# Kernel optimization log

Measured on AMD Instinct MI355X. Metric: run time of the kernel, lower is better.

## Reference

```python
import jax, jax.numpy as jnp
import numpy as np

N, D, H = 50000, 128, 2        # nodes, hidden_size(=ffn_size=out_channels), heads
E = 800000                      # edges
C = D                           # per-head out_channels (PyG TransformerConv)
EPS = 1e-5

def layer_norm(x, g, b):
    mu = jnp.mean(x, axis=-1, keepdims=True)
    var = jnp.mean((x - mu) ** 2, axis=-1, keepdims=True)
    return (x - mu) / jnp.sqrt(var + EPS) * g + b

def setup_inputs() -> dict:
    key = jax.random.key(0)
    ks = jax.random.split(key, 16)
    s_in = 1.0 / np.sqrt(D)
    s_ffn = 1.0 / np.sqrt(D)
    return {
        "x": jax.random.normal(ks[0], (N, D), jnp.float32),
        "edge_index": jax.random.randint(ks[1], (2, E), 0, N, jnp.int64),
        "ln1_g": jnp.ones((D,), jnp.float32),
        "ln1_b": jnp.zeros((D,), jnp.float32),
        "Wq": jax.random.normal(ks[2], (D, H * C), jnp.float32) * s_in,
        "bq": jnp.zeros((H * C,), jnp.float32),
        "Wk": jax.random.normal(ks[3], (D, H * C), jnp.float32) * s_in,
        "bk": jnp.zeros((H * C,), jnp.float32),
        "Wv": jax.random.normal(ks[4], (D, H * C), jnp.float32) * s_in,
        "bv": jnp.zeros((H * C,), jnp.float32),
        "Wskip": jax.random.normal(ks[5], (D, C), jnp.float32) * s_in,
        "bskip": jnp.zeros((C,), jnp.float32),
        "ln2_g": jnp.ones((D,), jnp.float32),
        "ln2_b": jnp.zeros((D,), jnp.float32),
        "W1": jax.random.normal(ks[6], (D, D), jnp.float32) * s_ffn,
        "b1": jnp.zeros((D,), jnp.float32),
        "W2": jax.random.normal(ks[7], (D, D), jnp.float32) * s_ffn,
        "b2": jnp.zeros((D,), jnp.float32),
    }

def reference(x, edge_index, ln1_g, ln1_b, Wq, bq, Wk, bk, Wv, bv,
              Wskip, bskip, ln2_g, ln2_b, W1, b1, W2, b2):
    src, dst = edge_index[0], edge_index[1]  # messages flow src(j) -> dst(i)
    n = x.shape[0]

    # --- self-attention block (pre-norm) ---
    y = layer_norm(x, ln1_g, ln1_b)
    q = (y @ Wq + bq).reshape(n, H, C)
    k = (y @ Wk + bk).reshape(n, H, C)
    v = (y @ Wv + bv).reshape(n, H, C)

    # per-edge attention logits [E, H]
    alpha = jnp.einsum('ehc,ehc->eh', q[dst], k[src]) / jnp.sqrt(jnp.float32(C))
    # softmax over incoming edges of each dst node
    m = jax.ops.segment_max(alpha, dst, num_segments=n)          # [N, H]
    p = jnp.exp(alpha - m[dst])                                  # [E, H]
    denom = jax.ops.segment_sum(p, dst, num_segments=n)          # [N, H]
    a = p / denom[dst]                                           # [E, H]

    attn = jax.ops.segment_sum(a[:, :, None] * v[src], dst, num_segments=n)  # [N,H,C]
    out = attn.mean(axis=1) + (y @ Wskip + bskip)  # concat=False mean + root skip
    x = x + out  # residual (dropout is identity at eval)

    # --- FFN block (pre-norm) ---
    h = layer_norm(x, ln2_g, ln2_b)
    h = jax.nn.gelu(h @ W1 + b1, approximate=False) @ W2 + b2
    return x + h
```

## Files before the change

kernel.cpp:

```cpp
#include <hip/hip_runtime.h>
#include <hip/hip_bf16.h>
#include <math.h>


typedef unsigned short u16;
using short8 = __attribute__((ext_vector_type(8))) short;
using f32x4  = __attribute__((ext_vector_type(4))) float;
using f32x2  = __attribute__((ext_vector_type(2))) float;

__device__ __forceinline__ float bf2f(u16 u) {
    return __uint_as_float(((unsigned int)u) << 16);
}
__device__ __forceinline__ u16 f2bf(float f) {
    __hip_bfloat16 h = __float2bfloat16(f);
    return __builtin_bit_cast(u16, h);
}
__device__ __forceinline__ float bfe(short8 v, int j) {
    return bf2f((u16)v[j]);
}
__device__ __forceinline__ void fp8x4_to_f32(int w, float* out) {
    f32x2 lo = __builtin_amdgcn_cvt_pk_f32_fp8(w, false);
    f32x2 hi = __builtin_amdgcn_cvt_pk_f32_fp8(w, true);
    out[0] = lo[0]; out[1] = lo[1]; out[2] = hi[0]; out[3] = hi[1];
}
__device__ __forceinline__ unsigned pack_fp8x4(float4 f) {
    unsigned w = 0;
    w = (unsigned)__builtin_amdgcn_cvt_pk_fp8_f32(f.x, f.y, (int)w, false);
    w = (unsigned)__builtin_amdgcn_cvt_pk_fp8_f32(f.z, f.w, (int)w, true);
    return w;
}

__global__ __launch_bounds__(256) void fused_prep_ln(
    const float* __restrict__ x, const float* __restrict__ ln1g,
    const float* __restrict__ ln1b,
    const float* __restrict__ Wq, const float* __restrict__ Wk,
    const float* __restrict__ Wv, const float* __restrict__ Ws,
    const float* __restrict__ W1, const float* __restrict__ W2,
    const float* __restrict__ bq, const float* __restrict__ bk,
    const float* __restrict__ bv, const float* __restrict__ bs,
    u16* __restrict__ wt, float* __restrict__ bc,
    u16* __restrict__ y, int* __restrict__ cnt, int n,
    const int* __restrict__ edst, int e, int histBlocks)
{
    if (blockIdx.x < (unsigned)histBlocks) {
        int stride = histBlocks * 256;
        for (int i = blockIdx.x * 256 + threadIdx.x; i < e; i += stride)
            atomicAdd(&cnt[edst[i]], 1);
        return;
    }
    int gsz = (gridDim.x - histBlocks) * 256;
    int gtid = (blockIdx.x - histBlocks) * 256 + threadIdx.x;

    for (int i = gtid; i < 147456 + 896; i += gsz) {
        if (i < 147456) {
            const float* W; int N; int base;
            if      (i <  32768) { W = Wq; N = 256; base = 0; }
            else if (i <  65536) { W = Wk; N = 256; base = 32768; }
            else if (i <  98304) { W = Wv; N = 256; base = 65536; }
            else if (i < 114688) { W = Ws; N = 128; base = 98304; }
            else if (i < 131072) { W = W1; N = 128; base = 114688; }
            else                 { W = W2; N = 128; base = 131072; }
            int j = i - base;
            int nIdx = j >> 7, k = j & 127;
            wt[i] = f2bf(W[(size_t)k * N + nIdx]);
        } else {
            int j = i - 147456;
            float v;
            if      (j < 256) v = bq[j];
            else if (j < 512) v = bk[j - 256];
            else if (j < 768) v = bv[j - 512];
            else              v = bs[j - 768];
            bc[j] = v;
        }
    }
    int lane = threadIdx.x & 63;
    int gw = gtid >> 6, nw = gsz >> 6;
    for (int row = gw; row < n; row += nw) {
        size_t base = (size_t)row * 128;
        float v0 = x[base + lane];
        float v1 = x[base + 64 + lane];
        float s1 = v0 + v1, s2 = v0 * v0 + v1 * v1;
        for (int o = 1; o <= 32; o <<= 1) {
            s1 += __shfl_xor(s1, o);
            s2 += __shfl_xor(s2, o);
        }
        float mu = s1 * (1.f / 128.f);
        float var = s2 * (1.f / 128.f) - mu * mu;
        float rstd = rsqrtf(var + 1e-5f);
        y[base + lane]      = f2bf((v0 - mu) * rstd * ln1g[lane] + ln1b[lane]);
        y[base + 64 + lane] = f2bf((v1 - mu) * rstd * ln1g[64 + lane] + ln1b[64 + lane]);
    }
}

__global__ __launch_bounds__(256) void scan_block_sum(const int* __restrict__ cnt,
                                                      int* __restrict__ bsum, int n) {
    __shared__ int s[256];
    int idx = blockIdx.x * 256 + threadIdx.x;
    s[threadIdx.x] = (idx < n) ? cnt[idx] : 0;
    __syncthreads();
    for (int o = 128; o > 0; o >>= 1) {
        if (threadIdx.x < o) s[threadIdx.x] += s[threadIdx.x + o];
        __syncthreads();
    }
    if (threadIdx.x == 0) bsum[blockIdx.x] = s[0];
}
__global__ __launch_bounds__(256) void scan_partials(const int* __restrict__ bsum,
                                                     int* __restrict__ bsumex, int nb) {
    __shared__ int s[256];
    int t = threadIdx.x;
    int v = (t < nb) ? bsum[t] : 0;
    s[t] = v;
    __syncthreads();
    for (int o = 1; o < 256; o <<= 1) {
        int add = (t >= o) ? s[t - o] : 0;
        __syncthreads();
        s[t] += add;
        __syncthreads();
    }
    bsumex[t] = s[t] - v;
}
__global__ __launch_bounds__(256) void scan_write(const int* __restrict__ cnt,
                                                  const int* __restrict__ bsumex,
                                                  int* __restrict__ rowptr,
                                                  int* __restrict__ cursor, int n, int etot) {
    __shared__ int s[256];
    int t = threadIdx.x;
    int idx = blockIdx.x * 256 + t;
    int v = (idx < n) ? cnt[idx] : 0;
    s[t] = v;
    __syncthreads();
    for (int o = 1; o < 256; o <<= 1) {
        int add = (t >= o) ? s[t - o] : 0;
        __syncthreads();
        s[t] += add;
        __syncthreads();
    }
    if (idx < n) {
        int ex = bsumex[blockIdx.x] + s[t] - v;
        rowptr[idx] = ex;
        cursor[idx] = ex;
    }
    if (idx == 0) rowptr[n] = etot;
}

__global__ __launch_bounds__(256, 3) void qkv_gemm(
    const u16* __restrict__ A, const u16* __restrict__ Bt,
    const float* __restrict__ bias, u16* __restrict__ qkv,
    float* __restrict__ skip, int n,
    const int* __restrict__ dst, const int* __restrict__ src,
    int* __restrict__ cursor, int* __restrict__ esrc, int e, int scatBlocks)
{
    __shared__ float wt4[4][32 * 66];
    if (blockIdx.x < (unsigned)scatBlocks) {
        int stride = scatBlocks * 256;
        for (int i = blockIdx.x * 256 + threadIdx.x; i < e; i += stride) {
            int p = atomicAdd(&cursor[dst[i]], 1);
            esrc[p] = src[i];
        }
        return;
    }
    int bid = blockIdx.x - scatBlocks;
    int wid = threadIdx.x >> 6, lane = threadIdx.x & 63;
    int wr = wid >> 1, wc = wid & 1;
    int r0 = bid * 64;
    int lm = lane & 15, quad = lane >> 4;
    float* wtile = wt4[wid];

    const u16* aBase = A + (size_t)(r0 + wr * 32 + lm) * 128 + quad * 8;
    short8 a0_0 = *(const short8*)(aBase + 0);
    short8 a0_1 = *(const short8*)(aBase + 32);
    short8 a0_2 = *(const short8*)(aBase + 64);
    short8 a0_3 = *(const short8*)(aBase + 96);
    short8 a1_0 = *(const short8*)(aBase + 16 * 128 + 0);
    short8 a1_1 = *(const short8*)(aBase + 16 * 128 + 32);
    short8 a1_2 = *(const short8*)(aBase + 16 * 128 + 64);
    short8 a1_3 = *(const short8*)(aBase + 16 * 128 + 96);

    int r = lane & 31, h = lane >> 5;
    int row = r0 + wr * 32 + r;
    bool rowOk = row < n;

    for (int by = 0; by < 7; ++by) {
        int c0 = by * 128;
        const u16* bBase = Bt + (size_t)(c0 + wc * 64 + lm) * 128 + quad * 8;
        f32x4 acc[2][4] = {};
#pragma unroll
        for (int kx = 0; kx < 4; ++kx) {
            short8 a0 = (kx == 0) ? a0_0 : (kx == 1) ? a0_1 : (kx == 2) ? a0_2 : a0_3;
            short8 a1 = (kx == 0) ? a1_0 : (kx == 1) ? a1_1 : (kx == 2) ? a1_2 : a1_3;
#pragma unroll
            for (int j = 0; j < 4; ++j) {
                short8 bj = *(const short8*)(bBase + (size_t)j * 16 * 128 + kx * 32);
                acc[0][j] = __builtin_amdgcn_mfma_f32_16x16x32_bf16(a0, bj, acc[0][j], 0, 0, 0);
                acc[1][j] = __builtin_amdgcn_mfma_f32_16x16x32_bf16(a1, bj, acc[1][j], 0, 0, 0);
            }
        }
#pragma unroll
        for (int j = 0; j < 4; ++j) {
            float bv = bias[c0 + wc * 64 + j * 16 + lm];
#pragma unroll
            for (int rt = 0; rt < 2; ++rt)
#pragma unroll
                for (int i2 = 0; i2 < 4; ++i2)
                    wtile[(rt * 16 + quad * 4 + i2) * 66 + j * 16 + lm]
                        = acc[rt][j][i2] + bv;
        }
        if (rowOk) {
            const float* wsrc = wtile + r * 66 + h * 32;
            int colW = wc * 64 + h * 32;
            if (c0 < 256) {
                u16* dp = qkv + (size_t)row * 640 + c0 + colW;
#pragma unroll
                for (int m2 = 0; m2 < 4; ++m2) {
                    short8 o;
#pragma unroll
                    for (int jj = 0; jj < 8; ++jj)
                        o[jj] = (short)f2bf(wsrc[m2 * 8 + jj]);
                    *(short8*)(dp + m2 * 8) = o;
                }
            } else if (c0 < 512) {
                unsigned char* kb = (unsigned char*)qkv + (size_t)row * 1280 + 512
                                    + (c0 - 256) + colW;
                uint4 w0, w1;
                w0.x = pack_fp8x4(make_float4(wsrc[0],  wsrc[1],  wsrc[2],  wsrc[3]));
                w0.y = pack_fp8x4(make_float4(wsrc[4],  wsrc[5],  wsrc[6],  wsrc[7]));
                w0.z = pack_fp8x4(make_float4(wsrc[8],  wsrc[9],  wsrc[10], wsrc[11]));
                w0.w = pack_fp8x4(make_float4(wsrc[12], wsrc[13], wsrc[14], wsrc[15]));
                w1.x = pack_fp8x4(make_float4(wsrc[16], wsrc[17], wsrc[18], wsrc[19]));
                w1.y = pack_fp8x4(make_float4(wsrc[20], wsrc[21], wsrc[22], wsrc[23]));
                w1.z = pack_fp8x4(make_float4(wsrc[24], wsrc[25], wsrc[26], wsrc[27]));
                w1.w = pack_fp8x4(make_float4(wsrc[28], wsrc[29], wsrc[30], wsrc[31]));
                *(uint4*)kb = w0;
                *(uint4*)(kb + 16) = w1;
            } else if (c0 < 768) {
                u16* dp = qkv + (size_t)row * 640 + 384 + (c0 - 512) + colW;
#pragma unroll
                for (int m2 = 0; m2 < 4; ++m2) {
                    short8 o;
#pragma unroll
                    for (int jj = 0; jj < 8; ++jj)
                        o[jj] = (short)f2bf(wsrc[m2 * 8 + jj]);
                    *(short8*)(dp + m2 * 8) = o;
                }
            } else {
                float* dp = skip + (size_t)row * 128 + colW;
#pragma unroll
                for (int m2 = 0; m2 < 8; ++m2)
                    *(float4*)(dp + m2 * 4) = *(const float4*)(wsrc + m2 * 4);
            }
        }
    }
}

__global__ __launch_bounds__(256) void attn_kernel(
    const u16* __restrict__ qkv, const int* __restrict__ rowptr,
    const int* __restrict__ esrc, const float* __restrict__ x,
    float* __restrict__ sx, const float* __restrict__ g2,
    const float* __restrict__ b2, u16* __restrict__ y, int n)
{
    int wid = threadIdx.x >> 6, lane = threadIdx.x & 63;
    int i = blockIdx.x * 4 + wid;
    if (i >= n) return;
    int slot = lane >> 5;
    int sub  = lane & 15;
    int colOff = ((lane >> 4) & 1) * 128 + sub * 8;

    const float scale = 0.08838834764831845f;
    short8 q8 = *(const short8*)(qkv + (size_t)i * 640 + colOff);
    float qf[8];
#pragma unroll
    for (int j = 0; j < 8; ++j) qf[j] = bfe(q8, j) * scale;

    int beg = rowptr[i], end = rowptr[i + 1];
    float l = 0.f;
    float acc[8] = {};

    int t = beg + slot;
    for (; t + 6 < end; t += 8) {
        int s0 = esrc[t], s1 = esrc[t + 2], s2 = esrc[t + 4], s3 = esrc[t + 6];
        const u16* n0 = qkv + (size_t)s0 * 640;
        const u16* n1 = qkv + (size_t)s1 * 640;
        const u16* n2 = qkv + (size_t)s2 * 640;
        const u16* n3 = qkv + (size_t)s3 * 640;
        uint2 kw0 = *(const uint2*)((const unsigned char*)(n0 + 256) + colOff);
        uint2 kw1 = *(const uint2*)((const unsigned char*)(n1 + 256) + colOff);
        uint2 kw2 = *(const uint2*)((const unsigned char*)(n2 + 256) + colOff);
        uint2 kw3 = *(const uint2*)((const unsigned char*)(n3 + 256) + colOff);
        short8 v0 = *(const short8*)(n0 + 384 + colOff);
        short8 v1 = *(const short8*)(n1 + 384 + colOff);
        short8 v2 = *(const short8*)(n2 + 384 + colOff);
        short8 v3 = *(const short8*)(n3 + 384 + colOff);
        float k0f[8], k1f[8], k2f[8], k3f[8];
        fp8x4_to_f32((int)kw0.x, k0f); fp8x4_to_f32((int)kw0.y, k0f + 4);
        fp8x4_to_f32((int)kw1.x, k1f); fp8x4_to_f32((int)kw1.y, k1f + 4);
        fp8x4_to_f32((int)kw2.x, k2f); fp8x4_to_f32((int)kw2.y, k2f + 4);
        fp8x4_to_f32((int)kw3.x, k3f); fp8x4_to_f32((int)kw3.y, k3f + 4);
        float d0 = 0.f, d1 = 0.f, d2 = 0.f, d3 = 0.f;
#pragma unroll
        for (int j = 0; j < 8; ++j) {
            d0 += qf[j] * k0f[j];
            d1 += qf[j] * k1f[j];
            d2 += qf[j] * k2f[j];
            d3 += qf[j] * k3f[j];
        }
#pragma unroll
        for (int o = 1; o <= 8; o <<= 1) {
            d0 += __shfl_xor(d0, o);
            d1 += __shfl_xor(d1, o);
            d2 += __shfl_xor(d2, o);
            d3 += __shfl_xor(d3, o);
        }
        float w0 = __expf(d0), w1 = __expf(d1);
        float w2 = __expf(d2), w3 = __expf(d3);
        l += w0 + w1 + w2 + w3;
#pragma unroll
        for (int j = 0; j < 8; ++j)
            acc[j] += w0 * bfe(v0, j) + w1 * bfe(v1, j)
                    + w2 * bfe(v2, j) + w3 * bfe(v3, j);
    }
    for (; t < end; t += 2) {
        int s0 = esrc[t];
        const u16* n0 = qkv + (size_t)s0 * 640;
        uint2 kw0 = *(const uint2*)((const unsigned char*)(n0 + 256) + colOff);
        short8 v0 = *(const short8*)(n0 + 384 + colOff);
        float k0f[8];
        fp8x4_to_f32((int)kw0.x, k0f); fp8x4_to_f32((int)kw0.y, k0f + 4);
        float d0 = 0.f;
#pragma unroll
        for (int j = 0; j < 8; ++j) d0 += qf[j] * k0f[j];
#pragma unroll
        for (int o = 1; o <= 8; o <<= 1) d0 += __shfl_xor(d0, o);
        float w0 = __expf(d0);
        l += w0;
#pragma unroll
        for (int j = 0; j < 8; ++j) acc[j] += w0 * bfe(v0, j);
    }

    l += __shfl_xor(l, 32);
    float inv = (l > 0.f) ? (1.f / l) : 0.f;
#pragma unroll
    for (int j = 0; j < 8; ++j) {
        acc[j] = (acc[j] + __shfl_xor(acc[j], 32)) * inv;
        acc[j] = 0.5f * (acc[j] + __shfl_xor(acc[j], 16));
    }

    if (lane < 16) {
        size_t base = (size_t)i * 128 + sub * 8;
        float4 xv0 = *(const float4*)(x + base);
        float4 xv1 = *(const float4*)(x + base + 4);
        float4 sk0 = *(const float4*)(sx + base);
        float4 sk1 = *(const float4*)(sx + base + 4);
        float r[8];
        r[0] = xv0.x + sk0.x + acc[0]; r[1] = xv0.y + sk0.y + acc[1];
        r[2] = xv0.z + sk0.z + acc[2]; r[3] = xv0.w + sk0.w + acc[3];
        r[4] = xv1.x + sk1.x + acc[4]; r[5] = xv1.y + sk1.y + acc[5];
        r[6] = xv1.z + sk1.z + acc[6]; r[7] = xv1.w + sk1.w + acc[7];
        *(float4*)(sx + base)     = make_float4(r[0], r[1], r[2], r[3]);
        *(float4*)(sx + base + 4) = make_float4(r[4], r[5], r[6], r[7]);
        float s1 = 0.f, s2 = 0.f;
#pragma unroll
        for (int j = 0; j < 8; ++j) { s1 += r[j]; s2 += r[j] * r[j]; }
#pragma unroll
        for (int o = 1; o <= 8; o <<= 1) {
            s1 += __shfl_xor(s1, o);
            s2 += __shfl_xor(s2, o);
        }
        float mu = s1 * (1.f / 128.f);
        float var = s2 * (1.f / 128.f) - mu * mu;
        float rstd = rsqrtf(var + 1e-5f);
        short8 o8;
#pragma unroll
        for (int j = 0; j < 8; ++j)
            o8[j] = (short)f2bf((r[j] - mu) * rstd * g2[sub * 8 + j] + b2[sub * 8 + j]);
        *(short8*)(y + base) = o8;
    }
}

__global__ __launch_bounds__(256) void ffn_kernel(
    const u16* __restrict__ y2, const u16* __restrict__ W1T,
    const float* __restrict__ b1, const u16* __restrict__ W2T,
    const float* __restrict__ b2, const float* __restrict__ x2,
    float* __restrict__ out, int n)
{
    __shared__ u16 t1[64 * 136];
    int wid = threadIdx.x >> 6, lane = threadIdx.x & 63;
    int lm = lane & 15, quad = lane >> 4;
    int r0 = blockIdx.x * 64 + wid * 16;

    const u16* aBase = y2 + (size_t)(r0 + lm) * 128 + quad * 8;
    f32x4 acc[8] = {};
#pragma unroll
    for (int kk = 0; kk < 128; kk += 32) {
        short8 a0 = *(const short8*)(aBase + kk);
#pragma unroll
        for (int j = 0; j < 8; ++j) {
            short8 bj = *(const short8*)(W1T + (size_t)(j * 16 + lm) * 128 + quad * 8 + kk);
            acc[j] = __builtin_amdgcn_mfma_f32_16x16x32_bf16(a0, bj, acc[j], 0, 0, 0);
        }
    }
#pragma unroll
    for (int j = 0; j < 8; ++j) {
        int col = j * 16 + lm;
        float bv = b1[col];
#pragma unroll
        for (int i2 = 0; i2 < 4; ++i2) {
            int rl = wid * 16 + quad * 4 + i2;
            float v = acc[j][i2] + bv;
            v = 0.5f * v * (1.f + erff(v * 0.70710678118654752f));
            t1[rl * 136 + col] = f2bf(v);
        }
    }
    __syncthreads();

    f32x4 acc2[8] = {};
#pragma unroll
    for (int kk = 0; kk < 128; kk += 32) {
        short8 a0 = *(const short8*)(t1 + (wid * 16 + lm) * 136 + quad * 8 + kk);
#pragma unroll
        for (int j = 0; j < 8; ++j) {
            short8 bj = *(const short8*)(W2T + (size_t)(j * 16 + lm) * 128 + quad * 8 + kk);
            acc2[j] = __builtin_amdgcn_mfma_f32_16x16x32_bf16(a0, bj, acc2[j], 0, 0, 0);
        }
    }
#pragma unroll
    for (int j = 0; j < 8; ++j) {
        int col = j * 16 + lm;
        float bv = b2[col];
#pragma unroll
        for (int i2 = 0; i2 < 4; ++i2) {
            int row = r0 + quad * 4 + i2;
            if (row >= n) continue;
            size_t ob = (size_t)row * 128 + col;
            out[ob] = acc2[j][i2] + bv + x2[ob];
        }
    }
}

extern "C" void kernel_launch(void* const* d_in, const int* in_sizes, int n_in,
                              void* d_out, int out_size, void* d_ws, size_t ws_size,
                              hipStream_t stream)
{
    const float* x    = (const float*)d_in[0];
    const int*   ei   = (const int*)d_in[1];

    int n = in_sizes[0] / 128;
    int e = in_sizes[1] / 2;
    const int* src  = ei;
    const int* dstp = ei + e;

    char* w = (char*)d_ws;
    size_t off = 0;
    auto alloc = [&](size_t bytes) -> void* {
        void* p = w + off;
        off = (off + bytes + 255) & ~(size_t)255;
        return p;
    };
    u16*   y    = (u16*)alloc((size_t)n * 128 * 2);
    u16*   qkv  = (u16*)alloc((size_t)n * 640 * 2);
    float* sx   = (float*)alloc((size_t)n * 128 * 4);
    u16*   wt   = (u16*)alloc((size_t)147456 * 2);
    float* bc   = (float*)alloc(896 * 4);
    int* cnt    = (int*)alloc((size_t)n * 4);
    int* cursor = (int*)alloc((size_t)n * 4);
    int* rowptr = (int*)alloc(((size_t)n + 1) * 4);
    int* esrc   = (int*)alloc((size_t)e * 4);
    int* bsum   = (int*)alloc(1024);
    int* bsumex = (int*)alloc(1024);

    int gr  = (n + 63) / 64;
    int nb  = (n + 255) / 256;
    int scatBlocks = 512;
    int histBlocks = 512;

    hipMemsetAsync(cnt, 0, (size_t)n * sizeof(int), stream);
    fused_prep_ln<<<2048 + histBlocks, 256, 0, stream>>>(
        x, (const float*)d_in[2], (const float*)d_in[3],
        (const float*)d_in[4], (const float*)d_in[6], (const float*)d_in[8],
        (const float*)d_in[10], (const float*)d_in[14], (const float*)d_in[16],
        (const float*)d_in[5], (const float*)d_in[7], (const float*)d_in[9],
        (const float*)d_in[11], wt, bc, y, cnt, n, dstp, e, histBlocks);
    scan_block_sum<<<nb, 256, 0, stream>>>(cnt, bsum, n);
    scan_partials<<<1, 256, 0, stream>>>(bsum, bsumex, nb);
    scan_write<<<nb, 256, 0, stream>>>(cnt, bsumex, rowptr, cursor, n, e);
    qkv_gemm<<<scatBlocks + gr, 256, 0, stream>>>(
        y, wt, bc, qkv, sx, n, dstp, src, cursor, esrc, e, scatBlocks);
    attn_kernel<<<(n + 3) / 4, 256, 0, stream>>>(qkv, rowptr, esrc, x, sx,
                                                 (const float*)d_in[12],
                                                 (const float*)d_in[13], y, n);
    ffn_kernel<<<gr, 256, 0, stream>>>(y, wt + 114688, (const float*)d_in[15],
                                       wt + 131072, (const float*)d_in[17],
                                       sx, (float*)d_out, n);
}
```

Measured before the change: 397.4 us.

## Stage A tile in LDS, bf16 epilogue tile, and unroll edge scatter in qkv_gemm

```diff
diff --git a/kernel.cpp b/kernel.cpp
--- a/kernel.cpp
+++ b/kernel.cpp
@@ -143,17 +143,30 @@
     if (idx == 0) rowptr[n] = etot;
 }
 
-__global__ __launch_bounds__(256, 3) void qkv_gemm(
+__global__ __launch_bounds__(256, 4) void qkv_gemm(
     const u16* __restrict__ A, const u16* __restrict__ Bt,
     const float* __restrict__ bias, u16* __restrict__ qkv,
     float* __restrict__ skip, int n,
     const int* __restrict__ dst, const int* __restrict__ src,
     int* __restrict__ cursor, int* __restrict__ esrc, int e, int scatBlocks)
 {
-    __shared__ float wt4[4][32 * 66];
+    __shared__ u16 ldsA[64 * 128];
+    __shared__ u16 epi[4][32 * 68];
     if (blockIdx.x < (unsigned)scatBlocks) {
         int stride = scatBlocks * 256;
-        for (int i = blockIdx.x * 256 + threadIdx.x; i < e; i += stride) {
+        int i = blockIdx.x * 256 + threadIdx.x;
+        for (; i + 3 * stride < e; i += 4 * stride) {
+            int d0 = dst[i],              s0 = src[i];
+            int d1 = dst[i + stride],     s1 = src[i + stride];
+            int d2 = dst[i + 2 * stride], s2 = src[i + 2 * stride];
+            int d3 = dst[i + 3 * stride], s3 = src[i + 3 * stride];
+            int p0 = atomicAdd(&cursor[d0], 1);
+            int p1 = atomicAdd(&cursor[d1], 1);
+            int p2 = atomicAdd(&cursor[d2], 1);
+            int p3 = atomicAdd(&cursor[d3], 1);
+            esrc[p0] = s0; esrc[p1] = s1; esrc[p2] = s2; esrc[p3] = s3;
+        }
+        for (; i < e; i += stride) {
             int p = atomicAdd(&cursor[dst[i]], 1);
             esrc[p] = src[i];
         }
@@ -164,21 +177,35 @@
     int wr = wid >> 1, wc = wid & 1;
     int r0 = bid * 64;
     int lm = lane & 15, quad = lane >> 4;
-    float* wtile = wt4[wid];
-
-    const u16* aBase = A + (size_t)(r0 + wr * 32 + lm) * 128 + quad * 8;
-    short8 a0_0 = *(const short8*)(aBase + 0);
-    short8 a0_1 = *(const short8*)(aBase + 32);
-    short8 a0_2 = *(const short8*)(aBase + 64);
-    short8 a0_3 = *(const short8*)(aBase + 96);
-    short8 a1_0 = *(const short8*)(aBase + 16 * 128 + 0);
-    short8 a1_1 = *(const short8*)(aBase + 16 * 128 + 32);
-    short8 a1_2 = *(const short8*)(aBase + 16 * 128 + 64);
-    short8 a1_3 = *(const short8*)(aBase + 16 * 128 + 96);
+
+    {
+        int t = threadIdx.x;
+#pragma unroll
+        for (int it = 0; it < 4; ++it) {
+            int s = it * 256 + t;
+            int q4  = s & 3;
+            int lmm = (s >> 2) & 15;
+            int kx  = (s >> 6) & 3;
+            int rt2 = (s >> 8) & 1;
+            int wr2 = (s >> 9) & 1;
+            int row = wr2 * 32 + rt2 * 16 + lmm;
+            int ucol = kx * 32 + q4 * 8;
+            int gRow = r0 + row;
+            if (gRow > n - 1) gRow = n - 1;
+            short8 val = *(const short8*)(A + (size_t)gRow * 128 + ucol);
+            *(short8*)(ldsA + (size_t)s * 8) = val;
+        }
+    }
+    __syncthreads();
+
+    int laneA = lm * 32 + quad * 8;
+    const u16* aB0 = ldsA + (wr * 2 + 0) * 2048 + laneA;
+    const u16* aB1 = ldsA + (wr * 2 + 1) * 2048 + laneA;
 
     int r = lane & 31, h = lane >> 5;
     int row = r0 + wr * 32 + r;
     bool rowOk = row < n;
+    u16* ep = epi[wid];
 
     for (int by = 0; by < 7; ++by) {
         int c0 = by * 128;
@@ -186,8 +213,8 @@
         f32x4 acc[2][4] = {};
 #pragma unroll
         for (int kx = 0; kx < 4; ++kx) {
-            short8 a0 = (kx == 0) ? a0_0 : (kx == 1) ? a0_1 : (kx == 2) ? a0_2 : a0_3;
-            short8 a1 = (kx == 0) ? a1_0 : (kx == 1) ? a1_1 : (kx == 2) ? a1_2 : a1_3;
+            short8 a0 = *(const short8*)(aB0 + kx * 512);
+            short8 a1 = *(const short8*)(aB1 + kx * 512);
 #pragma unroll
             for (int j = 0; j < 4; ++j) {
                 short8 bj = *(const short8*)(bBase + (size_t)j * 16 * 128 + kx * 32);
@@ -195,58 +222,74 @@
                 acc[1][j] = __builtin_amdgcn_mfma_f32_16x16x32_bf16(a1, bj, acc[1][j], 0, 0, 0);
             }
         }
-#pragma unroll
-        for (int j = 0; j < 4; ++j) {
-            float bv = bias[c0 + wc * 64 + j * 16 + lm];
-#pragma unroll
-            for (int rt = 0; rt < 2; ++rt)
-#pragma unroll
-                for (int i2 = 0; i2 < 4; ++i2)
-                    wtile[(rt * 16 + quad * 4 + i2) * 66 + j * 16 + lm]
-                        = acc[rt][j][i2] + bv;
-        }
-        if (rowOk) {
-            const float* wsrc = wtile + r * 66 + h * 32;
-            int colW = wc * 64 + h * 32;
-            if (c0 < 256) {
-                u16* dp = qkv + (size_t)row * 640 + c0 + colW;
-#pragma unroll
-                for (int m2 = 0; m2 < 4; ++m2) {
-                    short8 o;
-#pragma unroll
-                    for (int jj = 0; jj < 8; ++jj)
-                        o[jj] = (short)f2bf(wsrc[m2 * 8 + jj]);
-                    *(short8*)(dp + m2 * 8) = o;
+        if (c0 < 768) {
+#pragma unroll
+            for (int j = 0; j < 4; ++j) {
+                float bv = bias[c0 + wc * 64 + j * 16 + lm];
+#pragma unroll
+                for (int rt = 0; rt < 2; ++rt)
+#pragma unroll
+                    for (int i2 = 0; i2 < 4; ++i2)
+                        ep[(rt * 16 + quad * 4 + i2) * 68 + j * 16 + lm]
+                            = f2bf(acc[rt][j][i2] + bv);
+            }
+            if (rowOk) {
+                const u16* wsrc = ep + r * 68 + h * 32;
+                short8 w0 = *(const short8*)(wsrc + 0);
+                short8 w1 = *(const short8*)(wsrc + 8);
+                short8 w2 = *(const short8*)(wsrc + 16);
+                short8 w3 = *(const short8*)(wsrc + 24);
+                int colW = wc * 64 + h * 32;
+                if (c0 < 256) {
+                    u16* dp = qkv + (size_t)row * 640 + c0 + colW;
+                    *(short8*)(dp + 0)  = w0;
+                    *(short8*)(dp + 8)  = w1;
+                    *(short8*)(dp + 16) = w2;
+                    *(short8*)(dp + 24) = w3;
+                } else if (c0 < 512) {
+                    unsigned char* kb = (unsigned char*)qkv + (size_t)row * 1280
+                                        + 512 + (c0 - 256) + colW;
+                    uint4 o0, o1;
+                    o0.x = pack_fp8x4(make_float4(bfe(w0,0), bfe(w0,1), bfe(w0,2), bfe(w0,3)));
+                    o0.y = pack_fp8x4(make_float4(bfe(w0,4), bfe(w0,5), bfe(w0,6), bfe(w0,7)));
+                    o0.z = pack_fp8x4(make_float4(bfe(w1,0), bfe(w1,1), bfe(w1,2), bfe(w1,3)));
+                    o0.w = pack_fp8x4(make_float4(bfe(w1,4), bfe(w1,5), bfe(w1,6), bfe(w1,7)));
+                    o1.x = pack_fp8x4(make_float4(bfe(w2,0), bfe(w2,1), bfe(w2,2), bfe(w2,3)));
+                    o1.y = pack_fp8x4(make_float4(bfe(w2,4), bfe(w2,5), bfe(w2,6), bfe(w2,7)));
+                    o1.z = pack_fp8x4(make_float4(bfe(w3,0), bfe(w3,1), bfe(w3,2), bfe(w3,3)));
+                    o1.w = pack_fp8x4(make_float4(bfe(w3,4), bfe(w3,5), bfe(w3,6), bfe(w3,7)));
+                    *(uint4*)kb = o0;
+                    *(uint4*)(kb + 16) = o1;
+                } else {
+                    u16* dp = qkv + (size_t)row * 640 + 384 + (c0 - 512) + colW;
+                    *(short8*)(dp + 0)  = w0;
+                    *(short8*)(dp + 8)  = w1;
+                    *(short8*)(dp + 16) = w2;
+                    *(short8*)(dp + 24) = w3;
                 }
-            } else if (c0 < 512) {
-                unsigned char* kb = (unsigned char*)qkv + (size_t)row * 1280 + 512
-                                    + (c0 - 256) + colW;
-                uint4 w0, w1;
-                w0.x = pack_fp8x4(make_float4(wsrc[0],  wsrc[1],  wsrc[2],  wsrc[3]));
-                w0.y = pack_fp8x4(make_float4(wsrc[4],  wsrc[5],  wsrc[6],  wsrc[7]));
-                w0.z = pack_fp8x4(make_float4(wsrc[8],  wsrc[9],  wsrc[10], wsrc[11]));
-                w0.w = pack_fp8x4(make_float4(wsrc[12], wsrc[13], wsrc[14], wsrc[15]));
-                w1.x = pack_fp8x4(make_float4(wsrc[16], wsrc[17], wsrc[18], wsrc[19]));
-                w1.y = pack_fp8x4(make_float4(wsrc[20], wsrc[21], wsrc[22], wsrc[23]));
-                w1.z = pack_fp8x4(make_float4(wsrc[24], wsrc[25], wsrc[26], wsrc[27]));
-                w1.w = pack_fp8x4(make_float4(wsrc[28], wsrc[29], wsrc[30], wsrc[31]));
-                *(uint4*)kb = w0;
-                *(uint4*)(kb + 16) = w1;
-            } else if (c0 < 768) {
-                u16* dp = qkv + (size_t)row * 640 + 384 + (c0 - 512) + colW;
-#pragma unroll
-                for (int m2 = 0; m2 < 4; ++m2) {
-                    short8 o;
-#pragma unroll
-                    for (int jj = 0; jj < 8; ++jj)
-                        o[jj] = (short)f2bf(wsrc[m2 * 8 + jj]);
-                    *(short8*)(dp + m2 * 8) = o;
+            }
+        } else {
+            float* epF = (float*)ep;
+#pragma unroll
+            for (int hf = 0; hf < 2; ++hf) {
+#pragma unroll
+                for (int j2 = 0; j2 < 2; ++j2) {
+                    int j = hf * 2 + j2;
+                    float bv = bias[768 + wc * 64 + j * 16 + lm];
+#pragma unroll
+                    for (int rt = 0; rt < 2; ++rt)
+#pragma unroll
+                        for (int i2 = 0; i2 < 4; ++i2)
+                            epF[(rt * 16 + quad * 4 + i2) * 34 + j2 * 16 + lm]
+                                = acc[rt][j][i2] + bv;
                 }
-            } else {
-                float* dp = skip + (size_t)row * 128 + colW;
-#pragma unroll
-                for (int m2 = 0; m2 < 8; ++m2)
-                    *(float4*)(dp + m2 * 4) = *(const float4*)(wsrc + m2 * 4);
+                if (rowOk) {
+                    const float* ws = epF + r * 34 + h * 16;
+                    float* dp = skip + (size_t)row * 128 + wc * 64 + hf * 32 + h * 16;
+#pragma unroll
+                    for (int m2 = 0; m2 < 4; ++m2)
+                        *(float4*)(dp + m2 * 4) = *(const float4*)(ws + m2 * 4);
+                }
             }
         }
     }
@@ -469,7 +512,7 @@
 
     int gr  = (n + 63) / 64;
     int nb  = (n + 255) / 256;
-    int scatBlocks = 512;
+    int scatBlocks = 768;
     int histBlocks = 512;
 
     hipMemsetAsync(cnt, 0, (size_t)n * sizeof(int), stream);
```

Result: no change. 401.5 us (+1.0%).

## Shrink QKV GEMM tile to 32 rows and unroll edge scatter loop

Applied to the files above, without the earlier changes.

```diff
diff --git a/kernel.cpp b/kernel.cpp
--- a/kernel.cpp
+++ b/kernel.cpp
@@ -143,110 +143,121 @@
     if (idx == 0) rowptr[n] = etot;
 }
 
-__global__ __launch_bounds__(256, 3) void qkv_gemm(
+__global__ __launch_bounds__(256, 6) void qkv_gemm(
     const u16* __restrict__ A, const u16* __restrict__ Bt,
     const float* __restrict__ bias, u16* __restrict__ qkv,
     float* __restrict__ skip, int n,
     const int* __restrict__ dst, const int* __restrict__ src,
     int* __restrict__ cursor, int* __restrict__ esrc, int e, int scatBlocks)
 {
-    __shared__ float wt4[4][32 * 66];
+    __shared__ float epi[4][32 * 33];
     if (blockIdx.x < (unsigned)scatBlocks) {
         int stride = scatBlocks * 256;
-        for (int i = blockIdx.x * 256 + threadIdx.x; i < e; i += stride) {
+        int i = blockIdx.x * 256 + threadIdx.x;
+        for (; i + 3 * stride < e; i += 4 * stride) {
+            int d0 = dst[i],              s0 = src[i];
+            int d1 = dst[i + stride],     s1 = src[i + stride];
+            int d2 = dst[i + 2 * stride], s2 = src[i + 2 * stride];
+            int d3 = dst[i + 3 * stride], s3 = src[i + 3 * stride];
+            int p0 = atomicAdd(&cursor[d0], 1);
+            int p1 = atomicAdd(&cursor[d1], 1);
+            int p2 = atomicAdd(&cursor[d2], 1);
+            int p3 = atomicAdd(&cursor[d3], 1);
+            esrc[p0] = s0; esrc[p1] = s1; esrc[p2] = s2; esrc[p3] = s3;
+        }
+        for (; i < e; i += stride) {
             int p = atomicAdd(&cursor[dst[i]], 1);
             esrc[p] = src[i];
         }
         return;
     }
     int bid = blockIdx.x - scatBlocks;
-    int wid = threadIdx.x >> 6, lane = threadIdx.x & 63;
-    int wr = wid >> 1, wc = wid & 1;
-    int r0 = bid * 64;
+    int wc = threadIdx.x >> 6, lane = threadIdx.x & 63;
+    int r0 = bid * 32;
     int lm = lane & 15, quad = lane >> 4;
-    float* wtile = wt4[wid];
-
-    const u16* aBase = A + (size_t)(r0 + wr * 32 + lm) * 128 + quad * 8;
-    short8 a0_0 = *(const short8*)(aBase + 0);
-    short8 a0_1 = *(const short8*)(aBase + 32);
-    short8 a0_2 = *(const short8*)(aBase + 64);
-    short8 a0_3 = *(const short8*)(aBase + 96);
-    short8 a1_0 = *(const short8*)(aBase + 16 * 128 + 0);
-    short8 a1_1 = *(const short8*)(aBase + 16 * 128 + 32);
-    short8 a1_2 = *(const short8*)(aBase + 16 * 128 + 64);
-    short8 a1_3 = *(const short8*)(aBase + 16 * 128 + 96);
-
-    int r = lane & 31, h = lane >> 5;
-    int row = r0 + wr * 32 + r;
+
+    int ar0 = r0 + lm;       if (ar0 > n - 1) ar0 = n - 1;
+    int ar1 = r0 + 16 + lm;  if (ar1 > n - 1) ar1 = n - 1;
+    const u16* aB0 = A + (size_t)ar0 * 128 + quad * 8;
+    const u16* aB1 = A + (size_t)ar1 * 128 + quad * 8;
+    short8 a0_0 = *(const short8*)(aB0 + 0);
+    short8 a0_1 = *(const short8*)(aB0 + 32);
+    short8 a0_2 = *(const short8*)(aB0 + 64);
+    short8 a0_3 = *(const short8*)(aB0 + 96);
+    short8 a1_0 = *(const short8*)(aB1 + 0);
+    short8 a1_1 = *(const short8*)(aB1 + 32);
+    short8 a1_2 = *(const short8*)(aB1 + 64);
+    short8 a1_3 = *(const short8*)(aB1 + 96);
+    asm volatile("" : "+v"(a0_0), "+v"(a0_1), "+v"(a0_2), "+v"(a0_3),
+                      "+v"(a1_0), "+v"(a1_1), "+v"(a1_2), "+v"(a1_3));
+
+    int rr = lane & 31, hh = lane >> 5;
+    int row = r0 + rr;
     bool rowOk = row < n;
+    float* ep = epi[wc];
 
     for (int by = 0; by < 7; ++by) {
         int c0 = by * 128;
-        const u16* bBase = Bt + (size_t)(c0 + wc * 64 + lm) * 128 + quad * 8;
-        f32x4 acc[2][4] = {};
+        const u16* bBase = Bt + (size_t)(c0 + wc * 32 + lm) * 128 + quad * 8;
+        f32x4 acc[2][2] = {};
 #pragma unroll
         for (int kx = 0; kx < 4; ++kx) {
             short8 a0 = (kx == 0) ? a0_0 : (kx == 1) ? a0_1 : (kx == 2) ? a0_2 : a0_3;
             short8 a1 = (kx == 0) ? a1_0 : (kx == 1) ? a1_1 : (kx == 2) ? a1_2 : a1_3;
 #pragma unroll
-            for (int j = 0; j < 4; ++j) {
+            for (int j = 0; j < 2; ++j) {
                 short8 bj = *(const short8*)(bBase + (size_t)j * 16 * 128 + kx * 32);
                 acc[0][j] = __builtin_amdgcn_mfma_f32_16x16x32_bf16(a0, bj, acc[0][j], 0, 0, 0);
                 acc[1][j] = __builtin_amdgcn_mfma_f32_16x16x32_bf16(a1, bj, acc[1][j], 0, 0, 0);
             }
         }
 #pragma unroll
-        for (int j = 0; j < 4; ++j) {
-            float bv = bias[c0 + wc * 64 + j * 16 + lm];
+        for (int j = 0; j < 2; ++j) {
+            float bv = bias[c0 + wc * 32 + j * 16 + lm];
 #pragma unroll
             for (int rt = 0; rt < 2; ++rt)
 #pragma unroll
                 for (int i2 = 0; i2 < 4; ++i2)
-                    wtile[(rt * 16 + quad * 4 + i2) * 66 + j * 16 + lm]
+                    ep[(rt * 16 + quad * 4 + i2) * 33 + j * 16 + lm]
                         = acc[rt][j][i2] + bv;
         }
         if (rowOk) {
-            const float* wsrc = wtile + r * 66 + h * 32;
-            int colW = wc * 64 + h * 32;
+            const float* ws = ep + rr * 33 + hh * 16;
+            int colW = wc * 32 + hh * 16;
             if (c0 < 256) {
                 u16* dp = qkv + (size_t)row * 640 + c0 + colW;
-#pragma unroll
-                for (int m2 = 0; m2 < 4; ++m2) {
-                    short8 o;
-#pragma unroll
-                    for (int jj = 0; jj < 8; ++jj)
-                        o[jj] = (short)f2bf(wsrc[m2 * 8 + jj]);
-                    *(short8*)(dp + m2 * 8) = o;
+                short8 o0, o1;
+#pragma unroll
+                for (int jj = 0; jj < 8; ++jj) {
+                    o0[jj] = (short)f2bf(ws[jj]);
+                    o1[jj] = (short)f2bf(ws[8 + jj]);
                 }
+                *(short8*)(dp + 0) = o0;
+                *(short8*)(dp + 8) = o1;
             } else if (c0 < 512) {
-                unsigned char* kb = (unsigned char*)qkv + (size_t)row * 1280 + 512
-                                    + (c0 - 256) + colW;
-                uint4 w0, w1;
-                w0.x = pack_fp8x4(make_float4(wsrc[0],  wsrc[1],  wsrc[2],  wsrc[3]));
-                w0.y = pack_fp8x4(make_float4(wsrc[4],  wsrc[5],  wsrc[6],  wsrc[7]));
-                w0.z = pack_fp8x4(make_float4(wsrc[8],  wsrc[9],  wsrc[10], wsrc[11]));
-                w0.w = pack_fp8x4(make_float4(wsrc[12], wsrc[13], wsrc[14], wsrc[15]));
-                w1.x = pack_fp8x4(make_float4(wsrc[16], wsrc[17], wsrc[18], wsrc[19]));
-                w1.y = pack_fp8x4(make_float4(wsrc[20], wsrc[21], wsrc[22], wsrc[23]));
-                w1.z = pack_fp8x4(make_float4(wsrc[24], wsrc[25], wsrc[26], wsrc[27]));
-                w1.w = pack_fp8x4(make_float4(wsrc[28], wsrc[29], wsrc[30], wsrc[31]));
-                *(uint4*)kb = w0;
-                *(uint4*)(kb + 16) = w1;
+                unsigned char* kb = (unsigned char*)qkv + (size_t)row * 1280
+                                    + 512 + (c0 - 256) + colW;
+                uint4 o;
+                o.x = pack_fp8x4(make_float4(ws[0],  ws[1],  ws[2],  ws[3]));
+                o.y = pack_fp8x4(make_float4(ws[4],  ws[5],  ws[6],  ws[7]));
+                o.z = pack_fp8x4(make_float4(ws[8],  ws[9],  ws[10], ws[11]));
+                o.w = pack_fp8x4(make_float4(ws[12], ws[13], ws[14], ws[15]));
+                *(uint4*)kb = o;
             } else if (c0 < 768) {
                 u16* dp = qkv + (size_t)row * 640 + 384 + (c0 - 512) + colW;
-#pragma unroll
-                for (int m2 = 0; m2 < 4; ++m2) {
-                    short8 o;
-#pragma unroll
-                    for (int jj = 0; jj < 8; ++jj)
-                        o[jj] = (short)f2bf(wsrc[m2 * 8 + jj]);
-                    *(short8*)(dp + m2 * 8) = o;
+                short8 o0, o1;
+#pragma unroll
+                for (int jj = 0; jj < 8; ++jj) {
+                    o0[jj] = (short)f2bf(ws[jj]);
+                    o1[jj] = (short)f2bf(ws[8 + jj]);
                 }
+                *(short8*)(dp + 0) = o0;
+                *(short8*)(dp + 8) = o1;
             } else {
                 float* dp = skip + (size_t)row * 128 + colW;
 #pragma unroll
-                for (int m2 = 0; m2 < 8; ++m2)
-                    *(float4*)(dp + m2 * 4) = *(const float4*)(wsrc + m2 * 4);
+                for (int m2 = 0; m2 < 4; ++m2)
+                    *(float4*)(dp + m2 * 4) = *(const float4*)(ws + m2 * 4);
             }
         }
     }
@@ -467,8 +478,9 @@
     int* bsum   = (int*)alloc(1024);
     int* bsumex = (int*)alloc(1024);
 
-    int gr  = (n + 63) / 64;
-    int nb  = (n + 255) / 256;
+    int gr   = (n + 63) / 64;
+    int gr32 = (n + 31) / 32;
+    int nb   = (n + 255) / 256;
     int scatBlocks = 512;
     int histBlocks = 512;
 
@@ -482,7 +494,7 @@
     scan_block_sum<<<nb, 256, 0, stream>>>(cnt, bsum, n);
     scan_partials<<<1, 256, 0, stream>>>(bsum, bsumex, nb);
     scan_write<<<nb, 256, 0, stream>>>(cnt, bsumex, rowptr, cursor, n, e);
-    qkv_gemm<<<scatBlocks + gr, 256, 0, stream>>>(
+    qkv_gemm<<<scatBlocks + gr32, 256, 0, stream>>>(
         y, wt, bc, qkv, sx, n, dstp, src, cursor, esrc, e, scatBlocks);
     attn_kernel<<<(n + 3) / 4, 256, 0, stream>>>(qkv, rowptr, esrc, x, sx,
                                                  (const float*)d_in[12],
```

Measured after the change: 405.2 us. About the same (+2.0%).
